# Kernel optimization log

Measured on AMD Instinct MI355X. Metric: run time of the kernel, lower is better.

Reference implementation:

```python
import jax, jax.numpy as jnp
import numpy as np

T, R, L = 3, 4, 2            # node types, edge relations, HGT layers
H, D = 8, 16                 # heads, head dim
OUT = H * D                  # 128
IN = 128
N_T = 30000                  # nodes per type
E = 200000                   # edges per relation
EDGE_SRC = (0, 0, 1, 0)      # src node type of each relation
EDGE_DST = (0, 1, 0, 2)      # dst node type of each relation


def segment_softmax(logits, seg, num_seg):
    # softmax over edges grouped by destination node (per head)
    m = jax.ops.segment_max(logits, seg, num_segments=num_seg)
    m = jnp.where(jnp.isfinite(m), m, 0.0)
    e = jnp.exp(logits - m[seg])
    ssum = jax.ops.segment_sum(e, seg, num_segments=num_seg)
    return e / (ssum[seg] + 1e-16)


def hgt_layer(hs, edge_index, k_w, k_b, q_w, q_b, v_w, v_b, a_w, a_b, skip, a_rel, m_rel, p_rel):
    # per-node-type K/Q/V projections, [N_t, H, D]
    k = [(hs[t] @ k_w[t] + k_b[t]).reshape(-1, H, D) for t in range(T)]
    q = [(hs[t] @ q_w[t] + q_b[t]).reshape(-1, H, D) for t in range(T)]
    v = [(hs[t] @ v_w[t] + v_b[t]).reshape(-1, H, D) for t in range(T)]
    agg = [jnp.zeros((hs[t].shape[0], OUT), hs[t].dtype) for t in range(T)]
    inv_sqrt_d = 1.0 / np.sqrt(D).astype(np.float32)
    for r in range(R):
        s, d = EDGE_SRC[r], EDGE_DST[r]
        src, dst = edge_index[r, 0], edge_index[r, 1]
        # relation-specific transforms of source K and V
        k_rel = jnp.einsum('nhd,hde->nhe', k[s], a_rel[r])
        v_rel = jnp.einsum('nhd,hde->nhe', v[s], m_rel[r])
        k_j = k_rel[src]           # [E, H, D]
        v_j = v_rel[src]           # [E, H, D]
        q_i = q[d][dst]            # [E, H, D]
        logits = (q_i * k_j).sum(-1) * p_rel[r] * inv_sqrt_d   # [E, H]
        n_d = hs[d].shape[0]
        alpha = segment_softmax(logits, dst, n_d)              # [E, H]
        msg = (v_j * alpha[..., None]).reshape(-1, OUT)        # [E, OUT]
        agg[d] = agg[d] + jax.ops.segment_sum(msg, dst, num_segments=n_d)
    out = []
    for t in range(T):
        o = jax.nn.gelu(agg[t], approximate=False) @ a_w[t] + a_b[t]
        a_s = jax.nn.sigmoid(skip[t])
        out.append(a_s * o + (1.0 - a_s) * hs[t])   # learnable skip (dims match)
    return out


def _forward(x_t0, x_t1, x_t2, x_homo, lin_w, lin_b, k_w, k_b, q_w, q_b, v_w, v_b,
             a_w, a_b, skip, a_rel, m_rel, p_rel, edge_index, node_type_argmax):
    xs = [x_t0, x_t1, x_t2]
    # type-specific input projection + ReLU
    hs = [jax.nn.relu(xs[t] @ lin_w[t] + lin_b[t]) for t in range(T)]
    for l in range(L):
        hs = hgt_layer(hs, edge_index, k_w[l], k_b[l], q_w[l], q_b[l], v_w[l], v_b[l],
                       a_w[l], a_b[l], skip[l], a_rel[l], m_rel[l], p_rel[l])
    # hetero_to_homo_features: scatter per-type rows back to global node order
    num_nodes = x_homo.shape[0]
    h = jnp.zeros((num_nodes, OUT), hs[0].dtype)
    for t in range(T):
        mask = node_type_argmax == t
        local = jnp.clip(jnp.cumsum(mask) - 1, 0, hs[t].shape[0] - 1)
        h = jnp.where(mask[:, None], hs[t][local], h)
    return h


def setup_inputs() -> dict:
    key = jax.random.key(0)
    ks = jax.random.split(key, 16)
    w = 0.05
    return {
        'x_t0': jax.random.normal(ks[0], (N_T, IN), jnp.float32),
        'x_t1': jax.random.normal(ks[1], (N_T, IN), jnp.float32),
        'x_t2': jax.random.normal(ks[2], (N_T, IN), jnp.float32),
        'x_homo': jax.random.normal(ks[3], (T * N_T, IN), jnp.float32),
        'lin_w': jax.random.normal(ks[4], (T, IN, OUT), jnp.float32) * w,
        'lin_b': jnp.zeros((T, OUT), jnp.float32),
        'k_w': jax.random.normal(ks[5], (L, T, OUT, OUT), jnp.float32) * w,
        'k_b': jnp.zeros((L, T, OUT), jnp.float32),
        'q_w': jax.random.normal(ks[6], (L, T, OUT, OUT), jnp.float32) * w,
        'q_b': jnp.zeros((L, T, OUT), jnp.float32),
        'v_w': jax.random.normal(ks[7], (L, T, OUT, OUT), jnp.float32) * w,
        'v_b': jnp.zeros((L, T, OUT), jnp.float32),
        'a_w': jax.random.normal(ks[8], (L, T, OUT, OUT), jnp.float32) * w,
        'a_b': jnp.zeros((L, T, OUT), jnp.float32),
        'skip': jnp.ones((L, T), jnp.float32),
        'a_rel': jax.random.normal(ks[9], (L, R, H, D, D), jnp.float32) * 0.2,
        'm_rel': jax.random.normal(ks[10], (L, R, H, D, D), jnp.float32) * 0.2,
        'p_rel': jnp.ones((L, R, H), jnp.float32),
        'edge_index': jax.random.randint(ks[11], (R, 2, E), 0, N_T),
        'node_type_argmax': jnp.repeat(jnp.arange(T), N_T),
    }


def reference(x_t0, x_t1, x_t2, x_homo, lin_w, lin_b, k_w, k_b, q_w, q_b, v_w, v_b,
              a_w, a_b, skip, a_rel, m_rel, p_rel, edge_index, node_type_argmax):
    return _forward(x_t0, x_t1, x_t2, x_homo, lin_w, lin_b, k_w, k_b, q_w, q_b,
                    v_w, v_b, a_w, a_b, skip, a_rel, m_rel, p_rel,
                    edge_index, node_type_argmax)
```

## Files before the change

### kernel.cpp

```cpp
#include <hip/hip_runtime.h>
#include <math.h>

#define NT_NODES 30000
#define NE_EDGES 200000
#define NTY 3
#define NRL 4
#define NLY 2
#define NH 8
#define HD 16
#define FDIM 128
#define SCAN_BLOCKS 118

typedef unsigned short u16;
typedef unsigned int u32;
typedef __attribute__((ext_vector_type(8))) short bf16x8;
typedef __attribute__((ext_vector_type(4))) float f32x4;

__device__ __forceinline__ float bf2f(u16 u) {
  return __uint_as_float(((u32)u) << 16);
}
__device__ __forceinline__ u16 f2bf(float f) {
  u32 u = __float_as_uint(f);
  return (u16)((u + 0x7FFFu + ((u >> 16) & 1u)) >> 16);
}

__device__ __forceinline__ float gelu_f(float x) {
  return 0.5f * x * (1.f + erff(x * 0.7071067811865475f));
}

struct WtBatch { const float* w[23]; };
__global__ __launch_bounds__(256) void wt_prep(WtBatch wb, u16* wt) {
  const float* w = wb.w[blockIdx.x];
  u16* o = wt + (size_t)blockIdx.x * FDIM * FDIM;
  for (int i = threadIdx.x; i < FDIM * FDIM; i += 256) {
    int n = i >> 7, k = i & 127;
    o[i] = f2bf(w[(size_t)k * FDIM + n]);
  }
}

__global__ __launch_bounds__(256) void qfuse(const float* __restrict__ q_w,
                                             const float* __restrict__ q_b,
                                             const float* __restrict__ a_rel,
                                             const float* __restrict__ p_rel,
                                             u16* __restrict__ wqp,
                                             float* __restrict__ bqp) {
  const int lr = blockIdx.x;
  const int l = lr >> 2, r = lr & 3;
  const int dt = (r == 1) ? 1 : ((r == 3) ? 2 : 0);
  const float* qw = q_w + (size_t)(l * NTY + dt) * FDIM * FDIM;
  const float* qb = q_b + (size_t)(l * NTY + dt) * FDIM;
  const float* A  = a_rel + (size_t)(l * NRL + r) * NH * HD * HD;
  const float* pr = p_rel + (size_t)(l * NRL + r) * NH;
  u16* wo = wqp + (size_t)lr * FDIM * FDIM;
  float* bo = bqp + (size_t)lr * FDIM;

  __shared__ float As[NH * HD * HD];
  __shared__ float sh[NH];
  for (int i = threadIdx.x; i < NH * HD * HD; i += 256) As[i] = A[i];
  if (threadIdx.x < NH) sh[threadIdx.x] = pr[threadIdx.x] * 0.25f;
  __syncthreads();

  for (int i = threadIdx.x; i < FDIM * FDIM; i += 256) {
    int n = i >> 7, k = i & 127;
    int h = n >> 4, cl = n & 15;
    float s = 0.f;
    #pragma unroll
    for (int ee = 0; ee < HD; ee++)
      s += qw[(size_t)k * FDIM + h * HD + ee] * As[h * HD * HD + cl * HD + ee];
    wo[(size_t)n * FDIM + k] = f2bf(s * sh[h]);
  }
  if (threadIdx.x < FDIM) {
    int n = threadIdx.x, h = n >> 4, cl = n & 15;
    float s = 0.f;
    #pragma unroll
    for (int ee = 0; ee < HD; ee++)
      s += qb[h * HD + ee] * As[h * HD * HD + cl * HD + ee];
    bo[n] = s * sh[h];
  }
}


struct QkvOut { const u16* WT; const float* bias; u16* C; };
struct QkvTask {
  const u16* A; int nplain; QkvOut o[2];
  int haskv; const u16* WTk; const float* biask; const u16* WTv; const float* biasv; u32* Ckv;
};
struct QkvBatch { QkvTask t[3]; };

__global__ __launch_bounds__(256) void gemm_qkv(QkvBatch gb, int M) {
  const QkvTask tk = gb.t[blockIdx.z];
  const int tid = threadIdx.x;
  const int wv = tid >> 6;
  const int lane = tid & 63;
  const int row0 = blockIdx.x * 64;

  __shared__ u16 As[64 * 128];
  __shared__ u16 Bt[128 * 128];

  #pragma unroll
  for (int i = 0; i < 4; i++) {
    int g = tid + 256 * i;
    int r = g >> 4, k8 = g & 15;
    int grow = row0 + r;
    uint4 v = make_uint4(0, 0, 0, 0);
    if (grow < M) v = *(const uint4*)(tk.A + (size_t)grow * FDIM + k8 * 8);
    *(uint4*)(As + r * 128 + ((k8 ^ (r & 7)) * 8)) = v;
  }
  __syncthreads();

  const int rsel = lane & 15, ksel = lane >> 4;
  bf16x8 af[4][4];
  #pragma unroll
  for (int ks = 0; ks < 4; ks++) {
    int kg = ks * 4 + ksel;
    #pragma unroll
    for (int i = 0; i < 4; i++) {
      int r = 16 * i + rsel;
      af[ks][i] = *(const bf16x8*)(As + r * 128 + ((kg ^ (r & 7)) * 8));
    }
  }

  for (int ot = 0; ot < tk.nplain; ot++) {
    const QkvOut oo = tk.o[ot];
    #pragma unroll
    for (int i = 0; i < 8; i++) {
      int g = tid + 256 * i;
      int n = g >> 4, k8 = g & 15;
      uint4 v = *(const uint4*)(oo.WT + (size_t)n * FDIM + k8 * 8);
      *(uint4*)(Bt + n * 128 + ((k8 ^ (n & 7)) * 8)) = v;
    }
    __syncthreads();

    f32x4 acc[4][2] = {};
    #pragma unroll
    for (int ks = 0; ks < 4; ks++) {
      int kg = ks * 4 + ksel;
      bf16x8 bfr[2];
      #pragma unroll
      for (int j = 0; j < 2; j++) {
        int n = 32 * wv + 16 * j + rsel;
        bfr[j] = *(const bf16x8*)(Bt + n * 128 + ((kg ^ (n & 7)) * 8));
      }
      #pragma unroll
      for (int i = 0; i < 4; i++)
        #pragma unroll
        for (int j = 0; j < 2; j++)
          acc[i][j] = __builtin_amdgcn_mfma_f32_16x16x32_bf16(af[ks][i], bfr[j], acc[i][j], 0, 0, 0);
    }

    float bj[2];
    int colj[2];
    #pragma unroll
    for (int j = 0; j < 2; j++) {
      colj[j] = 32 * wv + 16 * j + rsel;
      bj[j] = oo.bias[colj[j]];
    }
    #pragma unroll
    for (int i = 0; i < 4; i++) {
      #pragma unroll
      for (int rr = 0; rr < 4; rr++) {
        int grow = row0 + 16 * i + (lane >> 4) * 4 + rr;
        if (grow >= M) continue;
        #pragma unroll
        for (int j = 0; j < 2; j++)
          oo.C[(size_t)grow * FDIM + colj[j]] = f2bf(acc[i][j][rr] + bj[j]);
      }
    }
    __syncthreads();
  }

  if (tk.haskv) {
    #pragma unroll
    for (int i = 0; i < 8; i++) {
      int g = tid + 256 * i;
      int n = g >> 4, k8 = g & 15;
      uint4 v = *(const uint4*)(tk.WTk + (size_t)n * FDIM + k8 * 8);
      *(uint4*)(Bt + n * 128 + ((k8 ^ (n & 7)) * 8)) = v;
    }
    __syncthreads();
    f32x4 accK[4][2] = {};
    #pragma unroll
    for (int ks = 0; ks < 4; ks++) {
      int kg = ks * 4 + ksel;
      bf16x8 bfr[2];
      #pragma unroll
      for (int j = 0; j < 2; j++) {
        int n = 32 * wv + 16 * j + rsel;
        bfr[j] = *(const bf16x8*)(Bt + n * 128 + ((kg ^ (n & 7)) * 8));
      }
      #pragma unroll
      for (int i = 0; i < 4; i++)
        #pragma unroll
        for (int j = 0; j < 2; j++)
          accK[i][j] = __builtin_amdgcn_mfma_f32_16x16x32_bf16(af[ks][i], bfr[j], accK[i][j], 0, 0, 0);
    }
    __syncthreads();
    #pragma unroll
    for (int i = 0; i < 8; i++) {
      int g = tid + 256 * i;
      int n = g >> 4, k8 = g & 15;
      uint4 v = *(const uint4*)(tk.WTv + (size_t)n * FDIM + k8 * 8);
      *(uint4*)(Bt + n * 128 + ((k8 ^ (n & 7)) * 8)) = v;
    }
    __syncthreads();
    f32x4 accV[4][2] = {};
    #pragma unroll
    for (int ks = 0; ks < 4; ks++) {
      int kg = ks * 4 + ksel;
      bf16x8 bfr[2];
      #pragma unroll
      for (int j = 0; j < 2; j++) {
        int n = 32 * wv + 16 * j + rsel;
        bfr[j] = *(const bf16x8*)(Bt + n * 128 + ((kg ^ (n & 7)) * 8));
      }
      #pragma unroll
      for (int i = 0; i < 4; i++)
        #pragma unroll
        for (int j = 0; j < 2; j++)
          accV[i][j] = __builtin_amdgcn_mfma_f32_16x16x32_bf16(af[ks][i], bfr[j], accV[i][j], 0, 0, 0);
    }

    float bk[2], bv[2];
    int colj[2];
    #pragma unroll
    for (int j = 0; j < 2; j++) {
      colj[j] = 32 * wv + 16 * j + rsel;
      bk[j] = tk.biask[colj[j]];
      bv[j] = tk.biasv[colj[j]];
    }
    #pragma unroll
    for (int i = 0; i < 4; i++) {
      #pragma unroll
      for (int rr = 0; rr < 4; rr++) {
        int grow = row0 + 16 * i + (lane >> 4) * 4 + rr;
        if (grow >= M) continue;
        #pragma unroll
        for (int j = 0; j < 2; j++) {
          u32 pk = (u32)f2bf(accK[i][j][rr] + bk[j]);
          u32 pv = (u32)f2bf(accV[i][j][rr] + bv[j]);
          tk.Ckv[(size_t)grow * FDIM + colj[j]] = pk | (pv << 16);
        }
      }
    }
  }
}

struct GemmTaskF {
  const float* A; const float* A2; const u16* WT; const float* bias;
  float* C; const u16* oldh; const float* skipp;
};
struct GemmBatchF { GemmTaskF t[3]; };

template<int GELU_A, int EPI_SKIP, int RELU, int BF16_OUT>
__global__ __launch_bounds__(256) void gemm_mfma_f(GemmBatchF gb, int M) {
  const GemmTaskF tk = gb.t[blockIdx.z];
  const int tid = threadIdx.x;
  const int wv = tid >> 6;
  const int lane = tid & 63;
  const int row0 = blockIdx.x * 64;

  __shared__ u16 As[64 * 128];
  __shared__ u16 Bt[128 * 128];

  #pragma unroll
  for (int i = 0; i < 4; i++) {
    int g = tid + 256 * i;
    int r = g >> 4, k8 = g & 15;
    int grow = row0 + r;
    float4 va = make_float4(0.f, 0.f, 0.f, 0.f), vb = va;
    if (grow < M) {
      const float* ap = tk.A + (size_t)grow * FDIM + k8 * 8;
      va = *(const float4*)ap;
      vb = *(const float4*)(ap + 4);
      if (GELU_A && tk.A2) {
        const float* ap2 = tk.A2 + (size_t)grow * FDIM + k8 * 8;
        float4 w = *(const float4*)ap2;
        float4 z = *(const float4*)(ap2 + 4);
        va.x += w.x; va.y += w.y; va.z += w.z; va.w += w.w;
        vb.x += z.x; vb.y += z.y; vb.z += z.z; vb.w += z.w;
      }
      if (GELU_A) {
        va.x = gelu_f(va.x); va.y = gelu_f(va.y); va.z = gelu_f(va.z); va.w = gelu_f(va.w);
        vb.x = gelu_f(vb.x); vb.y = gelu_f(vb.y); vb.z = gelu_f(vb.z); vb.w = gelu_f(vb.w);
      }
    }
    u32 w0 = (u32)f2bf(va.x) | ((u32)f2bf(va.y) << 16);
    u32 w1 = (u32)f2bf(va.z) | ((u32)f2bf(va.w) << 16);
    u32 w2 = (u32)f2bf(vb.x) | ((u32)f2bf(vb.y) << 16);
    u32 w3 = (u32)f2bf(vb.z) | ((u32)f2bf(vb.w) << 16);
    u32* dst = (u32*)(As + r * 128 + ((k8 ^ (r & 7)) * 8));
    dst[0] = w0; dst[1] = w1; dst[2] = w2; dst[3] = w3;
  }
  #pragma unroll
  for (int i = 0; i < 8; i++) {
    int g = tid + 256 * i;
    int n = g >> 4, k8 = g & 15;
    uint4 v = *(const uint4*)(tk.WT + (size_t)n * FDIM + k8 * 8);
    *(uint4*)(Bt + n * 128 + ((k8 ^ (n & 7)) * 8)) = v;
  }
  __syncthreads();

  f32x4 acc[4][2] = {};
  const int rsel = lane & 15, ksel = lane >> 4;
  #pragma unroll
  for (int ks = 0; ks < 4; ks++) {
    int kg = ks * 4 + ksel;
    bf16x8 af[4], bfr[2];
    #pragma unroll
    for (int i = 0; i < 4; i++) {
      int r = 16 * i + rsel;
      af[i] = *(const bf16x8*)(As + r * 128 + ((kg ^ (r & 7)) * 8));
    }
    #pragma unroll
    for (int j = 0; j < 2; j++) {
      int n = 32 * wv + 16 * j + rsel;
      bfr[j] = *(const bf16x8*)(Bt + n * 128 + ((kg ^ (n & 7)) * 8));
    }
    #pragma unroll
    for (int i = 0; i < 4; i++)
      #pragma unroll
      for (int j = 0; j < 2; j++)
        acc[i][j] = __builtin_amdgcn_mfma_f32_16x16x32_bf16(af[i], bfr[j], acc[i][j], 0, 0, 0);
  }

  float a_s = 0.f, b_s = 0.f;
  if (EPI_SKIP) { a_s = 1.f / (1.f + expf(-tk.skipp[0])); b_s = 1.f - a_s; }
  float bj[2];
  int colj[2];
  #pragma unroll
  for (int j = 0; j < 2; j++) {
    colj[j] = 32 * wv + 16 * j + rsel;
    bj[j] = tk.bias[colj[j]];
  }
  #pragma unroll
  for (int i = 0; i < 4; i++) {
    #pragma unroll
    for (int rr = 0; rr < 4; rr++) {
      int grow = row0 + 16 * i + (lane >> 4) * 4 + rr;
      if (grow >= M) continue;
      #pragma unroll
      for (int j = 0; j < 2; j++) {
        float v = acc[i][j][rr] + bj[j];
        if (RELU) v = fmaxf(v, 0.f);
        if (EPI_SKIP) v = a_s * v + b_s * bf2f(tk.oldh[(size_t)grow * FDIM + colj[j]]);
        if (BF16_OUT) ((u16*)tk.C)[(size_t)grow * FDIM + colj[j]] = f2bf(v);
        else tk.C[(size_t)grow * FDIM + colj[j]] = v;
      }
    }
  }
}

__global__ __launch_bounds__(256) void csr_hist(const int* __restrict__ edge_index,
                                                int* __restrict__ counts) {
  int idx = blockIdx.x * 256 + threadIdx.x;
  if (idx >= NRL * NE_EDGES) return;
  int r = idx / NE_EDGES, e = idx - r * NE_EDGES;
  int d = edge_index[(size_t)(r * 2 + 1) * NE_EDGES + e];
  atomicAdd(&counts[r * NT_NODES + d], 1);
}

__global__ __launch_bounds__(256) void scan_block(const int* __restrict__ counts,
                                                  int* __restrict__ off,
                                                  int* __restrict__ aux) {
  int r = blockIdx.y, b = blockIdx.x, t = threadIdx.x;
  int i = b * 256 + t;
  int v = (i < NT_NODES) ? counts[r * NT_NODES + i] : 0;
  __shared__ int lds[256];
  lds[t] = v;
  __syncthreads();
  #pragma unroll
  for (int dlt = 1; dlt < 256; dlt <<= 1) {
    int x = (t >= dlt) ? lds[t - dlt] : 0;
    __syncthreads();
    lds[t] += x;
    __syncthreads();
  }
  if (i < NT_NODES) off[(size_t)r * (NT_NODES + 1) + i] = lds[t] - v;
  if (t == 255) aux[r * SCAN_BLOCKS + b] = lds[255];
}

__global__ __launch_bounds__(128) void scan_aux(const int* __restrict__ aux,
                                                int* __restrict__ auxe,
                                                int* __restrict__ off) {
  int r = blockIdx.x, t = threadIdx.x;
  __shared__ int lds[128];
  int v = (t < SCAN_BLOCKS) ? aux[r * SCAN_BLOCKS + t] : 0;
  lds[t] = v;
  __syncthreads();
  #pragma unroll
  for (int dlt = 1; dlt < 128; dlt <<= 1) {
    int x = (t >= dlt) ? lds[t - dlt] : 0;
    __syncthreads();
    lds[t] += x;
    __syncthreads();
  }
  if (t < SCAN_BLOCKS) auxe[r * SCAN_BLOCKS + t] = lds[t] - v;
  if (t == 127) off[(size_t)r * (NT_NODES + 1) + NT_NODES] = lds[127];
}

__global__ __launch_bounds__(256) void scan_add(const int* __restrict__ auxe,
                                                int* __restrict__ off,
                                                int* __restrict__ cursor) {
  int r = blockIdx.y, b = blockIdx.x, t = threadIdx.x;
  int i = b * 256 + t;
  if (i >= NT_NODES) return;
  int val = off[(size_t)r * (NT_NODES + 1) + i] + auxe[r * SCAN_BLOCKS + b];
  off[(size_t)r * (NT_NODES + 1) + i] = val;
  cursor[r * NT_NODES + i] = val;
}

__global__ __launch_bounds__(256) void csr_scatter(const int* __restrict__ edge_index,
                                                   int* __restrict__ cursor,
                                                   int* __restrict__ csr_src) {
  int idx = blockIdx.x * 256 + threadIdx.x;
  if (idx >= NRL * NE_EDGES) return;
  int r = idx / NE_EDGES, e = idx - r * NE_EDGES;
  int s = edge_index[(size_t)(r * 2 + 0) * NE_EDGES + e];
  int d = edge_index[(size_t)(r * 2 + 1) * NE_EDGES + e];
  int pos = atomicAdd(&cursor[r * NT_NODES + d], 1);
  csr_src[(size_t)r * NE_EDGES + pos] = s;
}

__global__ void csr_pad(int* __restrict__ pad) {
  if (threadIdx.x < 8) pad[threadIdx.x] = 0;
}

struct AttnRel {
  const int* csr_src; const int* off;
  const u16* q;
  const u16* kv;
  const float* Mrel;
  float* agg;
};
struct AttnBatch { AttnRel r[4]; };

__global__ __launch_bounds__(256) void attn_fused(AttnBatch ab) {
  const AttnRel rp = ab.r[blockIdx.y];
  const int wave = threadIdx.x >> 6;
  const int lane = threadIdx.x & 63;
  const int d = blockIdx.x * 2 + (wave >> 1);
  if (d >= NT_NODES) return;
  const int hf = wave & 1;
  const int cl = lane & 15;
  const int gh = hf * 4 + (lane >> 4);
  const int grp = lane & ~15;
  const int el = lane & 7;

  float qp = bf2f(rp.q[(size_t)d * FDIM + hf * 64 + lane]);

  const u32* KV = (const u32*)rp.kv;
  const int* __restrict__ cs = rp.csr_src;
  int lo = rp.off[d], hi = rp.off[d + 1];
  lo = __builtin_amdgcn_readfirstlane(lo);
  hi = __builtin_amdgcn_readfirstlane(hi);
  const size_t poff = hf * 64 + lane;
  float acc = 0.f, ssum = 0.f;
  for (int pos = lo; pos < hi; pos += 8) {
    int s0 = cs[pos + 0], s1 = cs[pos + 1], s2 = cs[pos + 2], s3 = cs[pos + 3];
    int s4 = cs[pos + 4], s5 = cs[pos + 5], s6 = cs[pos + 6], s7 = cs[pos + 7];
    u32 w0 = KV[(size_t)s0 * 128 + poff], w1 = KV[(size_t)s1 * 128 + poff];
    u32 w2 = KV[(size_t)s2 * 128 + poff], w3 = KV[(size_t)s3 * 128 + poff];
    u32 w4 = KV[(size_t)s4 * 128 + poff], w5 = KV[(size_t)s5 * 128 + poff];
    u32 w6 = KV[(size_t)s6 * 128 + poff], w7 = KV[(size_t)s7 * 128 + poff];
    float p0 = qp * __uint_as_float(w0 << 16), p1 = qp * __uint_as_float(w1 << 16);
    float p2 = qp * __uint_as_float(w2 << 16), p3 = qp * __uint_as_float(w3 << 16);
    float p4 = qp * __uint_as_float(w4 << 16), p5 = qp * __uint_as_float(w5 << 16);
    float p6 = qp * __uint_as_float(w6 << 16), p7 = qp * __uint_as_float(w7 << 16);
    float s01 = (lane & 1) ? p0 : p1, c01 = (lane & 1) ? p1 : p0;
    float s23 = (lane & 1) ? p2 : p3, c23 = (lane & 1) ? p3 : p2;
    float s45 = (lane & 1) ? p4 : p5, c45 = (lane & 1) ? p5 : p4;
    float s67 = (lane & 1) ? p6 : p7, c67 = (lane & 1) ? p7 : p6;
    float r01 = c01 + __shfl_xor(s01, 1, 64);
    float r23 = c23 + __shfl_xor(s23, 1, 64);
    float r45 = c45 + __shfl_xor(s45, 1, 64);
    float r67 = c67 + __shfl_xor(s67, 1, 64);
    float sA = (lane & 2) ? r01 : r23, cA = (lane & 2) ? r23 : r01;
    float sB = (lane & 2) ? r45 : r67, cB = (lane & 2) ? r67 : r45;
    float rA = cA + __shfl_xor(sA, 2, 64);
    float rB = cB + __shfl_xor(sB, 2, 64);
    float sC = (lane & 4) ? rA : rB, cC = (lane & 4) ? rB : rA;
    float rF = cC + __shfl_xor(sC, 4, 64);
    rF += __shfl_xor(rF, 8, 64);
    int rem = hi - pos;
    float e = (el < rem) ? __expf(rF) : 0.f;
    float e0 = __shfl(e, grp + 0, 64), e1 = __shfl(e, grp + 1, 64);
    float e2 = __shfl(e, grp + 2, 64), e3 = __shfl(e, grp + 3, 64);
    float e4 = __shfl(e, grp + 4, 64), e5 = __shfl(e, grp + 5, 64);
    float e6 = __shfl(e, grp + 6, 64), e7 = __shfl(e, grp + 7, 64);
    acc += e0 * __uint_as_float(w0 & 0xFFFF0000u) + e1 * __uint_as_float(w1 & 0xFFFF0000u)
         + e2 * __uint_as_float(w2 & 0xFFFF0000u) + e3 * __uint_as_float(w3 & 0xFFFF0000u)
         + e4 * __uint_as_float(w4 & 0xFFFF0000u) + e5 * __uint_as_float(w5 & 0xFFFF0000u)
         + e6 * __uint_as_float(w6 & 0xFFFF0000u) + e7 * __uint_as_float(w7 & 0xFFFF0000u);
    ssum += ((e0 + e1) + (e2 + e3)) + ((e4 + e5) + (e6 + e7));
  }
  float inv = 1.f / (ssum + 1e-16f);
  float S = acc * inv;

  const float* M = rp.Mrel + (size_t)gh * 256;
  float o = 0.f;
  #pragma unroll
  for (int d2 = 0; d2 < 16; d2++) {
    float sv = __shfl(S, grp + d2, 64);
    o += sv * M[d2 * 16 + cl];
  }
  rp.agg[(size_t)d * FDIM + hf * 64 + lane] = o;
}

__global__ __launch_bounds__(256) void scatter_out(const float* h0, const float* h1,
                                                   const float* h2, const int* ntype,
                                                   float* out, int NN) {
  int idx = blockIdx.x * 256 + threadIdx.x;
  if (idx >= NN * 32) return;
  int i = idx >> 5, c4 = idx & 31;
  int t = ntype[i];
  const float* hp = (t == 0) ? h0 : ((t == 1) ? h1 : h2);
  int local = i - t * NT_NODES;
  ((float4*)out)[idx] = ((const float4*)hp)[(size_t)local * 32 + c4];
}

static const int ESRC[NRL] = {0, 0, 1, 0};
static const int EDST[NRL] = {0, 1, 0, 2};

extern "C" void kernel_launch(void* const* d_in, const int* in_sizes, int n_in,
                              void* d_out, int out_size, void* d_ws, size_t ws_size,
                              hipStream_t stream) {
  const float* x[3] = {(const float*)d_in[0], (const float*)d_in[1], (const float*)d_in[2]};
  const float* lin_w = (const float*)d_in[4];
  const float* lin_b = (const float*)d_in[5];
  const float* k_w   = (const float*)d_in[6];
  const float* k_b   = (const float*)d_in[7];
  const float* q_w   = (const float*)d_in[8];
  const float* q_b   = (const float*)d_in[9];
  const float* v_w   = (const float*)d_in[10];
  const float* v_b   = (const float*)d_in[11];
  const float* a_w   = (const float*)d_in[12];
  const float* a_b   = (const float*)d_in[13];
  const float* skip  = (const float*)d_in[14];
  const float* a_rel = (const float*)d_in[15];
  const float* m_rel = (const float*)d_in[16];
  const float* p_rel = (const float*)d_in[17];
  const int* edge_index = (const int*)d_in[18];
  const int* ntype   = (const int*)d_in[19];
  float* out = (float*)d_out;

  const size_t NF = (size_t)NT_NODES * FDIM;
  float* p = (float*)d_ws;
  auto alloc = [&](size_t n) { float* r = p; p += n; return r; };
  float* bufA = alloc(3 * NF);
  float* bufB = alloc(3 * NF);
  float* agg  = alloc(3 * NF);
  float* aggX = alloc(NF);
  u16* kv0 = (u16*)alloc(NF);
  u16* kv1 = (u16*)alloc(NF);
  u16* wt  = (u16*)alloc(23 * FDIM * FDIM / 2);
  u16* wqp = (u16*)alloc(8 * FDIM * FDIM / 2);
  float* bqp = alloc(8 * FDIM);
  int* counts  = (int*)(p);
  int* cursor  = counts + NRL * NT_NODES;
  int* offsets = cursor + NRL * NT_NODES;
  int* aux     = offsets + NRL * (NT_NODES + 1);
  int* auxe    = aux + NRL * SCAN_BLOCKS;
  int* csr_src = auxe + NRL * SCAN_BLOCKS;

  const int gemm_gx = (NT_NODES + 63) / 64;

  {
    WtBatch wb{};
    for (int l = 0; l < NLY; l++) {
      for (int t = 0; t < 3; t++)
        wb.w[l * 7 + t] = q_w + (size_t)(l * NTY + t) * FDIM * FDIM;
      wb.w[l * 7 + 3] = k_w + (size_t)(l * NTY + 0) * FDIM * FDIM;
      wb.w[l * 7 + 4] = v_w + (size_t)(l * NTY + 0) * FDIM * FDIM;
      wb.w[l * 7 + 5] = k_w + (size_t)(l * NTY + 1) * FDIM * FDIM;
      wb.w[l * 7 + 6] = v_w + (size_t)(l * NTY + 1) * FDIM * FDIM;
    }
    for (int t = 0; t < 3; t++)
      wb.w[14 + t] = lin_w + (size_t)t * FDIM * FDIM;
    for (int l = 0; l < NLY; l++)
      for (int t = 0; t < 3; t++)
        wb.w[17 + l * 3 + t] = a_w + (size_t)(l * NTY + t) * FDIM * FDIM;
    wt_prep<<<dim3(23), 256, 0, stream>>>(wb, wt);
    qfuse<<<dim3(NLY * NRL), 256, 0, stream>>>(q_w, q_b, a_rel, p_rel, wqp, bqp);
  }

  hipMemsetAsync(counts, 0, NRL * NT_NODES * sizeof(int), stream);
  csr_hist<<<dim3((NRL * NE_EDGES + 255) / 256), 256, 0, stream>>>(edge_index, counts);
  scan_block<<<dim3(SCAN_BLOCKS, NRL), 256, 0, stream>>>(counts, offsets, aux);
  scan_aux<<<dim3(NRL), 128, 0, stream>>>(aux, auxe, offsets);
  scan_add<<<dim3(SCAN_BLOCKS, NRL), 256, 0, stream>>>(auxe, offsets, cursor);
  csr_scatter<<<dim3((NRL * NE_EDGES + 255) / 256), 256, 0, stream>>>(edge_index, cursor, csr_src);
  csr_pad<<<dim3(1), 64, 0, stream>>>(csr_src + (size_t)NRL * NE_EDGES);

  {
    GemmBatchF gb{};
    for (int t = 0; t < 3; t++) {
      gb.t[t].A = x[t];
      gb.t[t].A2 = nullptr;
      gb.t[t].WT = wt + (size_t)(14 + t) * FDIM * FDIM;
      gb.t[t].bias = lin_b + (size_t)t * FDIM;
      gb.t[t].C = (float*)((u16*)bufA + (size_t)t * NF);
      gb.t[t].oldh = nullptr; gb.t[t].skipp = nullptr;
    }
    gemm_mfma_f<0, 0, 1, 1><<<dim3(gemm_gx, 1, 3), 256, 0, stream>>>(gb, NT_NODES);
  }

  float* cur = bufA;
  float* alt = bufB;
  for (int l = 0; l < NLY; l++) {
    u16* qbf = (u16*)alt;
    const u16* hb = (const u16*)cur;

    {
      QkvBatch gb{};
      gb.t[0].A = hb;  gb.t[0].nplain = 2;
      gb.t[0].o[0] = { wqp + (size_t)(l * 4 + 0) * FDIM * FDIM, bqp + (size_t)(l * 4 + 0) * FDIM, qbf + 0 * NF };
      gb.t[0].o[1] = { wqp + (size_t)(l * 4 + 2) * FDIM * FDIM, bqp + (size_t)(l * 4 + 2) * FDIM, qbf + 2 * NF };
      gb.t[0].haskv = 1;
      gb.t[0].WTk = wt + (size_t)(l * 7 + 3) * FDIM * FDIM;
      gb.t[0].biask = k_b + (size_t)(l * NTY + 0) * FDIM;
      gb.t[0].WTv = wt + (size_t)(l * 7 + 4) * FDIM * FDIM;
      gb.t[0].biasv = v_b + (size_t)(l * NTY + 0) * FDIM;
      gb.t[0].Ckv = (u32*)kv0;
      gb.t[1].A = hb + NF;  gb.t[1].nplain = 1;
      gb.t[1].o[0] = { wqp + (size_t)(l * 4 + 1) * FDIM * FDIM, bqp + (size_t)(l * 4 + 1) * FDIM, qbf + 1 * NF };
      gb.t[1].haskv = 1;
      gb.t[1].WTk = wt + (size_t)(l * 7 + 5) * FDIM * FDIM;
      gb.t[1].biask = k_b + (size_t)(l * NTY + 1) * FDIM;
      gb.t[1].WTv = wt + (size_t)(l * 7 + 6) * FDIM * FDIM;
      gb.t[1].biasv = v_b + (size_t)(l * NTY + 1) * FDIM;
      gb.t[1].Ckv = (u32*)kv1;
      gb.t[2].A = hb + 2 * NF;  gb.t[2].nplain = 1;
      gb.t[2].o[0] = { wqp + (size_t)(l * 4 + 3) * FDIM * FDIM, bqp + (size_t)(l * 4 + 3) * FDIM, qbf + 3 * NF };
      gb.t[2].haskv = 0;
      gemm_qkv<<<dim3(gemm_gx, 1, 3), 256, 0, stream>>>(gb, NT_NODES);
    }

    {
      AttnBatch ab{};
      for (int r = 0; r < NRL; r++) {
        ab.r[r].csr_src = csr_src + (size_t)r * NE_EDGES;
        ab.r[r].off  = offsets + (size_t)r * (NT_NODES + 1);
        ab.r[r].q    = qbf + (size_t)r * NF;
        ab.r[r].kv   = (ESRC[r] == 0) ? kv0 : kv1;
        ab.r[r].Mrel = m_rel + (size_t)(l * NRL + r) * NH * HD * HD;
        ab.r[r].agg  = (r == 2) ? aggX : (agg + (size_t)EDST[r] * NF);
      }
      attn_fused<<<dim3((NT_NODES + 1) / 2, NRL), 256, 0, stream>>>(ab);
    }

    {
      GemmBatchF gb{};
      for (int t = 0; t < 3; t++) {
        gb.t[t].A = agg + (size_t)t * NF;
        gb.t[t].A2 = (t == 0) ? aggX : nullptr;
        gb.t[t].WT = wt + (size_t)(17 + l * 3 + t) * FDIM * FDIM;
        gb.t[t].bias = a_b + (size_t)(l * NTY + t) * FDIM;
        gb.t[t].oldh = hb + (size_t)t * NF;
        gb.t[t].skipp = skip + (size_t)(l * NTY + t);
        if (l == 0) gb.t[t].C = (float*)((u16*)alt + (size_t)t * NF);
        else        gb.t[t].C = alt + (size_t)t * NF;
      }
      if (l == 0) gemm_mfma_f<1, 1, 0, 1><<<dim3(gemm_gx, 1, 3), 256, 0, stream>>>(gb, NT_NODES);
      else        gemm_mfma_f<1, 1, 0, 0><<<dim3(gemm_gx, 1, 3), 256, 0, stream>>>(gb, NT_NODES);
    }
    float* tmp = cur; cur = alt; alt = tmp;
  }

  const int NN = 3 * NT_NODES;
  scatter_out<<<dim3((NN * 32 + 255) / 256), 256, 0, stream>>>(
      cur, cur + NF, cur + 2 * NF, ntype, out, NN);
}
```

Baseline: 525.6 us.

## Store attention aggregates in bf16 and split type-0 QKV GEMM across extra grid slice

The attention kernel now writes its per-relation aggregation outputs as bf16 instead of fp32, and the output projection GEMM gains a BF16_A template path that reads bf16 aggregates (summing the extra relation-2 buffer and applying GELU) directly into shared memory. This halves the write and read traffic of the aggregate buffers. Separately, the type-0 task of the QKV GEMM, which produced two Q outputs, is split so the second Q projection runs as a fourth grid-z slice, balancing work across blocks at the cost of re-reading the type-0 activations. The bf16 aggregates add rounding before GELU.

New measurement: 533.8 us. About the same (+1.6%).

```diff
diff --git a/kernel.cpp b/kernel.cpp
--- a/kernel.cpp
+++ b/kernel.cpp
@@ -85,7 +85,7 @@
   const u16* A; int nplain; QkvOut o[2];
   int haskv; const u16* WTk; const float* biask; const u16* WTv; const float* biasv; u32* Ckv;
 };
-struct QkvBatch { QkvTask t[3]; };
+struct QkvBatch { QkvTask t[4]; };
 
 __global__ __launch_bounds__(256) void gemm_qkv(QkvBatch gb, int M) {
   const QkvTask tk = gb.t[blockIdx.z];
@@ -251,7 +251,7 @@
 };
 struct GemmBatchF { GemmTaskF t[3]; };
 
-template<int GELU_A, int EPI_SKIP, int RELU, int BF16_OUT>
+template<int GELU_A, int EPI_SKIP, int RELU, int BF16_OUT, int BF16_A>
 __global__ __launch_bounds__(256) void gemm_mfma_f(GemmBatchF gb, int M) {
   const GemmTaskF tk = gb.t[blockIdx.z];
   const int tid = threadIdx.x;
@@ -267,29 +267,48 @@
     int g = tid + 256 * i;
     int r = g >> 4, k8 = g & 15;
     int grow = row0 + r;
-    float4 va = make_float4(0.f, 0.f, 0.f, 0.f), vb = va;
-    if (grow < M) {
-      const float* ap = tk.A + (size_t)grow * FDIM + k8 * 8;
-      va = *(const float4*)ap;
-      vb = *(const float4*)(ap + 4);
-      if (GELU_A && tk.A2) {
-        const float* ap2 = tk.A2 + (size_t)grow * FDIM + k8 * 8;
-        float4 w = *(const float4*)ap2;
-        float4 z = *(const float4*)(ap2 + 4);
-        va.x += w.x; va.y += w.y; va.z += w.z; va.w += w.w;
-        vb.x += z.x; vb.y += z.y; vb.z += z.z; vb.w += z.w;
-      }
-      if (GELU_A) {
-        va.x = gelu_f(va.x); va.y = gelu_f(va.y); va.z = gelu_f(va.z); va.w = gelu_f(va.w);
-        vb.x = gelu_f(vb.x); vb.y = gelu_f(vb.y); vb.z = gelu_f(vb.z); vb.w = gelu_f(vb.w);
-      }
-    }
-    u32 w0 = (u32)f2bf(va.x) | ((u32)f2bf(va.y) << 16);
-    u32 w1 = (u32)f2bf(va.z) | ((u32)f2bf(va.w) << 16);
-    u32 w2 = (u32)f2bf(vb.x) | ((u32)f2bf(vb.y) << 16);
-    u32 w3 = (u32)f2bf(vb.z) | ((u32)f2bf(vb.w) << 16);
-    u32* dst = (u32*)(As + r * 128 + ((k8 ^ (r & 7)) * 8));
-    dst[0] = w0; dst[1] = w1; dst[2] = w2; dst[3] = w3;
+    if (BF16_A) {
+      uint4 v = make_uint4(0, 0, 0, 0);
+      if (grow < M) {
+        v = *(const uint4*)((const u16*)tk.A + (size_t)grow * FDIM + k8 * 8);
+        if (GELU_A) {
+          uint4 v2 = make_uint4(0, 0, 0, 0);
+          if (tk.A2) v2 = *(const uint4*)((const u16*)tk.A2 + (size_t)grow * FDIM + k8 * 8);
+          u32 vv[4] = {v.x, v.y, v.z, v.w};
+          u32 ww[4] = {v2.x, v2.y, v2.z, v2.w};
+          #pragma unroll
+          for (int q = 0; q < 4; q++) {
+            float lo = __uint_as_float(vv[q] << 16);
+            float hi = __uint_as_float(vv[q] & 0xFFFF0000u);
+            if (tk.A2) {
+              lo += __uint_as_float(ww[q] << 16);
+              hi += __uint_as_float(ww[q] & 0xFFFF0000u);
+            }
+            lo = gelu_f(lo); hi = gelu_f(hi);
+            vv[q] = (u32)f2bf(lo) | ((u32)f2bf(hi) << 16);
+          }
+          v = make_uint4(vv[0], vv[1], vv[2], vv[3]);
+        }
+      }
+      *(uint4*)(As + r * 128 + ((k8 ^ (r & 7)) * 8)) = v;
+    } else {
+      float4 va = make_float4(0.f, 0.f, 0.f, 0.f), vb = va;
+      if (grow < M) {
+        const float* ap = tk.A + (size_t)grow * FDIM + k8 * 8;
+        va = *(const float4*)ap;
+        vb = *(const float4*)(ap + 4);
+        if (GELU_A) {
+          va.x = gelu_f(va.x); va.y = gelu_f(va.y); va.z = gelu_f(va.z); va.w = gelu_f(va.w);
+          vb.x = gelu_f(vb.x); vb.y = gelu_f(vb.y); vb.z = gelu_f(vb.z); vb.w = gelu_f(vb.w);
+        }
+      }
+      u32 w0 = (u32)f2bf(va.x) | ((u32)f2bf(va.y) << 16);
+      u32 w1 = (u32)f2bf(va.z) | ((u32)f2bf(va.w) << 16);
+      u32 w2 = (u32)f2bf(vb.x) | ((u32)f2bf(vb.y) << 16);
+      u32 w3 = (u32)f2bf(vb.z) | ((u32)f2bf(vb.w) << 16);
+      u32* dst = (u32*)(As + r * 128 + ((k8 ^ (r & 7)) * 8));
+      dst[0] = w0; dst[1] = w1; dst[2] = w2; dst[3] = w3;
+    }
   }
   #pragma unroll
   for (int i = 0; i < 8; i++) {
@@ -430,7 +449,7 @@
   const u16* q;
   const u16* kv;
   const float* Mrel;
-  float* agg;
+  u16* agg;
 };
 struct AttnBatch { AttnRel r[4]; };
 
@@ -503,7 +522,7 @@
     float sv = __shfl(S, grp + d2, 64);
     o += sv * M[d2 * 16 + cl];
   }
-  rp.agg[(size_t)d * FDIM + hf * 64 + lane] = o;
+  rp.agg[(size_t)d * FDIM + hf * 64 + lane] = f2bf(o);
 }
 
 __global__ __launch_bounds__(256) void scatter_out(const float* h0, const float* h1,
@@ -548,8 +567,8 @@
   auto alloc = [&](size_t n) { float* r = p; p += n; return r; };
   float* bufA = alloc(3 * NF);
   float* bufB = alloc(3 * NF);
-  float* agg  = alloc(3 * NF);
-  float* aggX = alloc(NF);
+  u16* aggb = (u16*)alloc(3 * NF / 2);
+  u16* aggXb = (u16*)alloc(NF / 2);
   u16* kv0 = (u16*)alloc(NF);
   u16* kv1 = (u16*)alloc(NF);
   u16* wt  = (u16*)alloc(23 * FDIM * FDIM / 2);
@@ -601,7 +620,7 @@
       gb.t[t].C = (float*)((u16*)bufA + (size_t)t * NF);
       gb.t[t].oldh = nullptr; gb.t[t].skipp = nullptr;
     }
-    gemm_mfma_f<0, 0, 1, 1><<<dim3(gemm_gx, 1, 3), 256, 0, stream>>>(gb, NT_NODES);
+    gemm_mfma_f<0, 0, 1, 1, 0><<<dim3(gemm_gx, 1, 3), 256, 0, stream>>>(gb, NT_NODES);
   }
 
   float* cur = bufA;
@@ -612,9 +631,8 @@
 
     {
       QkvBatch gb{};
-      gb.t[0].A = hb;  gb.t[0].nplain = 2;
+      gb.t[0].A = hb;  gb.t[0].nplain = 1;
       gb.t[0].o[0] = { wqp + (size_t)(l * 4 + 0) * FDIM * FDIM, bqp + (size_t)(l * 4 + 0) * FDIM, qbf + 0 * NF };
-      gb.t[0].o[1] = { wqp + (size_t)(l * 4 + 2) * FDIM * FDIM, bqp + (size_t)(l * 4 + 2) * FDIM, qbf + 2 * NF };
       gb.t[0].haskv = 1;
       gb.t[0].WTk = wt + (size_t)(l * 7 + 3) * FDIM * FDIM;
       gb.t[0].biask = k_b + (size_t)(l * NTY + 0) * FDIM;
@@ -632,7 +650,10 @@
       gb.t[2].A = hb + 2 * NF;  gb.t[2].nplain = 1;
       gb.t[2].o[0] = { wqp + (size_t)(l * 4 + 3) * FDIM * FDIM, bqp + (size_t)(l * 4 + 3) * FDIM, qbf + 3 * NF };
       gb.t[2].haskv = 0;
-      gemm_qkv<<<dim3(gemm_gx, 1, 3), 256, 0, stream>>>(gb, NT_NODES);
+      gb.t[3].A = hb;  gb.t[3].nplain = 1;
+      gb.t[3].o[0] = { wqp + (size_t)(l * 4 + 2) * FDIM * FDIM, bqp + (size_t)(l * 4 + 2) * FDIM, qbf + 2 * NF };
+      gb.t[3].haskv = 0;
+      gemm_qkv<<<dim3(gemm_gx, 1, 4), 256, 0, stream>>>(gb, NT_NODES);
     }
 
     {
@@ -643,7 +664,7 @@
         ab.r[r].q    = qbf + (size_t)r * NF;
         ab.r[r].kv   = (ESRC[r] == 0) ? kv0 : kv1;
         ab.r[r].Mrel = m_rel + (size_t)(l * NRL + r) * NH * HD * HD;
-        ab.r[r].agg  = (r == 2) ? aggX : (agg + (size_t)EDST[r] * NF);
+        ab.r[r].agg  = (r == 2) ? aggXb : (aggb + (size_t)EDST[r] * NF);
       }
       attn_fused<<<dim3((NT_NODES + 1) / 2, NRL), 256, 0, stream>>>(ab);
     }
@@ -651,8 +672,8 @@
     {
       GemmBatchF gb{};
       for (int t = 0; t < 3; t++) {
-        gb.t[t].A = agg + (size_t)t * NF;
-        gb.t[t].A2 = (t == 0) ? aggX : nullptr;
+        gb.t[t].A = (const float*)(aggb + (size_t)t * NF);
+        gb.t[t].A2 = (t == 0) ? (const float*)aggXb : nullptr;
         gb.t[t].WT = wt + (size_t)(17 + l * 3 + t) * FDIM * FDIM;
         gb.t[t].bias = a_b + (size_t)(l * NTY + t) * FDIM;
         gb.t[t].oldh = hb + (size_t)t * NF;
@@ -660,8 +681,8 @@
         if (l == 0) gb.t[t].C = (float*)((u16*)alt + (size_t)t * NF);
         else        gb.t[t].C = alt + (size_t)t * NF;
       }
-      if (l == 0) gemm_mfma_f<1, 1, 0, 1><<<dim3(gemm_gx, 1, 3), 256, 0, stream>>>(gb, NT_NODES);
-      else        gemm_mfma_f<1, 1, 0, 0><<<dim3(gemm_gx, 1, 3), 256, 0, stream>>>(gb, NT_NODES);
+      if (l == 0) gemm_mfma_f<1, 1, 0, 1, 1><<<dim3(gemm_gx, 1, 3), 256, 0, stream>>>(gb, NT_NODES);
+      else        gemm_mfma_f<1, 1, 0, 0, 1><<<dim3(gemm_gx, 1, 3), 256, 0, stream>>>(gb, NT_NODES);
     }
     float* tmp = cur; cur = alt; alt = tmp;
   }
```
